# Optimization experiments

Measured on AMD Instinct MI355X. Metric: run time of the kernel, lower is better.

## Reference

```python
import jax, jax.numpy as jnp
import numpy as np

N = 40000          # nodes
E = 640000         # edges (avg degree 16)
F_IN = 128         # num_node_features
H = 64             # hidden_channels
C_OUT = 32         # num_classes


def _glorot(key, fan_in, fan_out):
    lim = np.sqrt(6.0 / (fan_in + fan_out)).astype(np.float32)
    return jax.random.uniform(key, (fan_in, fan_out), jnp.float32, -lim, lim)


def setup_inputs() -> dict:
    key = jax.random.key(0)
    ks = jax.random.split(key, 12)
    x = jax.random.normal(ks[0], (N, F_IN), jnp.float32)
    edge_index = jax.random.randint(ks[1], (2, E), 0, N, dtype=jnp.int32)
    batch = jnp.zeros((N,), jnp.int32)  # unused by forward, kept for signature fidelity
    return {
        "x": x,
        "edge_index": edge_index,
        "batch": batch,
        "W1": _glorot(ks[2], F_IN, H),      "b1": jnp.zeros((H,), jnp.float32),
        "W2": _glorot(ks[3], H, 2 * H),     "b2": jnp.zeros((2 * H,), jnp.float32),
        "W3": _glorot(ks[4], 2 * H, 2 * H), "b3": jnp.zeros((2 * H,), jnp.float32),
        "W4": _glorot(ks[5], 2 * H, H),     "b4": jnp.zeros((H,), jnp.float32),
        "Wl": _glorot(ks[6], H, C_OUT),     "bl": jnp.zeros((C_OUT,), jnp.float32),
    }


def _gcn_norm(edge_index, n_nodes):
    """Add self-loops and compute symmetric D^{-1/2} A D^{-1/2} edge weights."""
    loop = jnp.arange(n_nodes, dtype=edge_index.dtype)
    src = jnp.concatenate([edge_index[0], loop])
    dst = jnp.concatenate([edge_index[1], loop])
    deg = jax.ops.segment_sum(jnp.ones_like(dst, dtype=jnp.float32), dst,
                              num_segments=n_nodes)
    d_inv_sqrt = jnp.where(deg > 0, jax.lax.rsqrt(deg), 0.0)
    norm = d_inv_sqrt[src] * d_inv_sqrt[dst]  # [E + N]
    return src, dst, norm


def _gcn_conv(h, W, b, src, dst, norm, n_nodes):
    h = h @ W                                   # [N, d_out] linear transform first
    msg = h[src] * norm[:, None]                # gather + edge scaling
    agg = jax.ops.segment_sum(msg, dst, num_segments=n_nodes)  # scatter-add
    return agg + b


def reference(x, edge_index, batch, W1, b1, W2, b2, W3, b3, W4, b4, Wl, bl):
    n_nodes = x.shape[0]
    src, dst, norm = _gcn_norm(edge_index, n_nodes)
    # eval mode: F.dropout(training=False) is identity
    h = jax.nn.relu(_gcn_conv(x, W1, b1, src, dst, norm, n_nodes))
    h = jax.nn.relu(_gcn_conv(h, W2, b2, src, dst, norm, n_nodes))
    h = jax.nn.relu(_gcn_conv(h, W3, b3, src, dst, norm, n_nodes))
    h = jax.nn.relu(_gcn_conv(h, W4, b4, src, dst, norm, n_nodes))
    return h @ Wl + bl  # [N, C_OUT]
```

## Files before the change

### kernel.cpp

```cpp
#include <hip/hip_runtime.h>
#include <hip/hip_bf16.h>


using bf16x8 = __attribute__((ext_vector_type(8))) __bf16;
using f32x4  = __attribute__((ext_vector_type(4))) float;

#define BUKCAP 8192

__device__ __forceinline__ int block_detect_bf16(const unsigned short* __restrict__ x16) {
    __shared__ int cnt;
    if (threadIdx.x == 0) cnt = 0;
    __syncthreads();
    if (threadIdx.x < 128) {
        unsigned e = (x16[2 * threadIdx.x] >> 7) & 0xFF;
        if (e >= 100 && e <= 135) atomicAdd(&cnt, 1);
    }
    __syncthreads();
    return cnt >= 64;
}

struct PrepDesc { const void* src; void* dst; int n; int mode; int dol2; int strideK; };
struct PrepArgs { PrepDesc d[12]; int pre[13]; int ndesc; };

__global__ __launch_bounds__(256) void prep_stage(PrepArgs a,
// ... 8 lines not shown
    const int npre = a.pre[a.ndesc];
    if (b >= npre) {
        __shared__ int hist[160], start[160], run[160];
        const int t = threadIdx.x;
        const int base = (b - npre) * 2048;
        int sv[8], dv[8];
        #pragma unroll
        for (int j = 0; j < 8; ++j) {
            int e = base + j * 256 + t;
            if (e < E) { sv[j] = src[e]; dv[j] = dst[e]; } else dv[j] = -1;
        }
        if (t < NBUK) { hist[t] = 0; run[t] = 0; }
        __syncthreads();
        #pragma unroll
        for (int j = 0; j < 8; ++j)
            if (dv[j] >= 0) atomicAdd(&hist[dv[j] >> 8], 1);
        __syncthreads();
        if (t < NBUK && hist[t] > 0)
            start[t] = atomicAdd(&bukFill[t], hist[t]);
        __syncthreads();
        #pragma unroll
        for (int j = 0; j < 8; ++j) {
            if (dv[j] >= 0) {
                int bk = dv[j] >> 8;
                int slot = start[bk] + atomicAdd(&run[bk], 1);
                staging[(size_t)bk * BUKCAP + slot] = ((unsigned)dv[j] << 16) | (unsigned)sv[j];
            }
        }
        return;
    }
    const int fl = block_detect_bf16(x16);
    if (b == 0 && threadIdx.x == 0) *flagG = fl;
    int s = 0;
    for (; s < a.ndesc - 1; ++s) if (b < a.pre[s + 1]) break;
    const PrepDesc d = a.d[s];
    int i = (b - a.pre[s]) * 256 + threadIdx.x;
    if (i >= d.n) return;
    float v = fl ? __bfloat162float(((const __hip_bfloat16*)d.src)[i])
                 : ((const float*)d.src)[i];
    if (d.mode == 0) {
        ((float*)d.dst)[i] = v;
    } else {
        int k = i >> d.dol2;
        int col = i & ((1 << d.dol2) - 1);
        ((__hip_bfloat16*)d.dst)[col * d.strideK + k] = __float2bfloat16(v);
    }
}

template<int NTPW, bool RAW_A>
__device__ __forceinline__ void gemm_core(const void* __restrict__ Ain,
                                          const __hip_bfloat16* __restrict__ WT,
                                          __hip_bfloat16* __restrict__ out,
                                          int d_in, int d_out_log2, int strideK,
                                          bool bfmode, int blk, int tid) {
    const int wave = tid >> 6, lane = tid & 63;
    const int m = lane & 15, quad = lane >> 4;
    const int rowBase = blk * 64;
    const int nkc = d_in >> 5;
    const int nt0 = wave * NTPW;

    f32x4 acc[4][NTPW];
    #pragma unroll
    for (int rt = 0; rt < 4; ++rt)
        #pragma unroll
        for (int j = 0; j < NTPW; ++j)
            acc[rt][j] = (f32x4){0.f, 0.f, 0.f, 0.f};

    auto mainloop = [&](bool asBF) {
        for (int kc = 0; kc < nkc; ++kc) {
            const int koff = (kc << 5) + quad * 8;
            bf16x8 a[4];
            #pragma unroll
            for (int rt = 0; rt < 4; ++rt) {
                const size_t off = (size_t)(rowBase + rt * 16 + m) * d_in + koff;
                if (!RAW_A || asBF) {
                    a[rt] = *(const bf16x8*)((const __hip_bfloat16*)Ain + off);
                } else {
                    const float* p = (const float*)Ain + off;
                    float4 f0 = *(const float4*)p;
                    float4 f1 = *(const float4*)(p + 4);
                    union { bf16x8 v; __hip_bfloat16 h[8]; } u;
                    u.h[0] = __float2bfloat16(f0.x); u.h[1] = __float2bfloat16(f0.y);
                    u.h[2] = __float2bfloat16(f0.z); u.h[3] = __float2bfloat16(f0.w);
                    u.h[4] = __float2bfloat16(f1.x); u.h[5] = __float2bfloat16(f1.y);
                    u.h[6] = __float2bfloat16(f1.z); u.h[7] = __float2bfloat16(f1.w);
                    a[rt] = u.v;
                }
            }
            #pragma unroll
            for (int j = 0; j < NTPW; ++j) {
                const int n = ((nt0 + j) << 4) + m;
                bf16x8 b = *(const bf16x8*)&WT[n * strideK + koff];
                #pragma unroll
                for (int rt = 0; rt < 4; ++rt)
                    acc[rt][j] = __builtin_amdgcn_mfma_f32_16x16x32_bf16(a[rt], b, acc[rt][j], 0, 0, 0);
            }
        }
    };
    if (bfmode) mainloop(true); else mainloop(false);

    const int d_out = 1 << d_out_log2;
    #pragma unroll
    for (int rt = 0; rt < 4; ++rt) {
        const int row = rowBase + rt * 16 + quad * 4;
        #pragma unroll
        for (int j = 0; j < NTPW; ++j) {
            const int col = ((nt0 + j) << 4) + m;
            #pragma unroll
            for (int r = 0; r < 4; ++r)
                out[(size_t)(row + r) * d_out + col] = __float2bfloat16(acc[rt][j][r]);
        }
    }
}

__global__ __launch_bounds__(256) void scatter_gemm(const unsigned* __restrict__ staging,
                                                    const int* __restrict__ bukFill,
                                                    float* __restrict__ dinvA,
                                                    int2* __restrict__ nodeInfo,
                                                    unsigned short* __restrict__ csr16,
                                                    int N, int NBUK,
                                                    const void* __restrict__ x,
                                                    const __hip_bfloat16* __restrict__ WT0,
                                                    __hip_bfloat16* __restrict__ lin1,
                                                    int strideK0,
                                                    const int* __restrict__ flag,
                                                    __hip_bfloat16* __restrict__ TbufS,
                                                    __hip_bfloat16* __restrict__ HbufS) {
    if ((int)blockIdx.x < NBUK) {
        __shared__ int cur[256];
        const int t = threadIdx.x;
        const int i = (blockIdx.x << 8) + t;
        cur[t] = i * 64;
        if ((int)blockIdx.x == NBUK - 1) {
            if (i == N) dinvA[N] = 0.f;
            unsigned* z1 = (unsigned*)(TbufS + (size_t)N * 64);
            unsigned* z2 = (unsigned*)(TbufS + (size_t)N * 128);
            unsigned* z3 = (unsigned*)(HbufS + (size_t)N * 64);
            if (t < 32) z1[t] = 0u;
            else if (t < 96) z2[t - 32] = 0u;
            else if (t < 128) z3[t - 96] = 0u;
        }
        __syncthreads();
        const int fill = bukFill[blockIdx.x];
        const unsigned* st = staging + (size_t)blockIdx.x * BUKCAP;
        for (int k = t; k < fill; k += 256) {
            unsigned u = st[k];
            int pos = atomicAdd(&cur[(u >> 16) & 255], 1);
            csr16[pos] = (unsigned short)(u & 0xffffu);
        }
        __syncthreads();
        const int c = cur[t] - i * 64;
        const int cp = (c + 7) & ~7;
        if (i < N) {
            const float dv = rsqrtf((float)(c + 1));
            nodeInfo[i] = make_int2(__float_as_int(dv), cp);
            dinvA[i] = dv;
        }
        const int e1 = i * 64 + cp;
        for (int p = cur[t]; p < e1; ++p) csr16[p] = (unsigned short)N;
        return;
    }
    gemm_core<1, true>(x, WT0, lin1, 128, 6, strideK0,
                       (*flag != 0), blockIdx.x - NBUK, threadIdx.x);
}

template<int W>
__device__ __forceinline__ float gather_acc8w(const __hip_bfloat16* __restrict__ Hin,
                                              int cb, int node,
                                              const int2* __restrict__ nodeInfo,
                                              const unsigned short* __restrict__ csr16,
                                              const float* __restrict__ dinvA,
                                              float acc[8]) {
    const __hip_bfloat16* base = Hin + cb;
    const unsigned short* wp = csr16 + (size_t)node * 64;
    uint4 ix0 = *(const uint4*)(wp);
    uint4 ix1 = *(const uint4*)(wp + 8);
    const uint4 selfv = *(const uint4*)(base + (size_t)node * W);
    const int2 info = nodeInfo[node];
    const float di = __int_as_float(info.x);
    const int cp = info.y;
    auto loadrow = [&](unsigned s) -> uint4 {
        return *(const uint4*)(base + (size_t)s * W);
    };
    auto accumw = [&](uint4 v, float w) {
        union { uint4 q; __hip_bfloat162 h2[4]; } c;
        c.q = v;
        #pragma unroll
        for (int j = 0; j < 4; ++j) {
            float2 p = __bfloat1622float2(c.h2[j]);
            acc[2 * j]     += w * p.x;
            acc[2 * j + 1] += w * p.y;
        }
    };
    #pragma unroll
    for (int j = 0; j < 8; ++j) acc[j] = 0.f;
    accumw(selfv, di);
    int e = 0;
    uint4 cu = ix0, nx = ix1;
    while (e < cp) {
        const unsigned s0 = cu.x & 0xffffu, s1 = cu.x >> 16;
        const unsigned s2 = cu.y & 0xffffu, s3 = cu.y >> 16;
        const unsigned s4 = cu.z & 0xffffu, s5 = cu.z >> 16;
        const unsigned s6 = cu.w & 0xffffu, s7 = cu.w >> 16;
        uint4 r0 = loadrow(s0), r1 = loadrow(s1), r2 = loadrow(s2), r3 = loadrow(s3);
        uint4 r4 = loadrow(s4), r5 = loadrow(s5), r6 = loadrow(s6), r7 = loadrow(s7);
        float w0 = dinvA[s0], w1 = dinvA[s1], w2 = dinvA[s2], w3 = dinvA[s3];
        float w4 = dinvA[s4], w5 = dinvA[s5], w6 = dinvA[s6], w7 = dinvA[s7];
        uint4 pf = (e + 16 < cp) ? *(const uint4*)(wp + e + 16) : nx;
        accumw(r0, w0); accumw(r1, w1); accumw(r2, w2); accumw(r3, w3);
        accumw(r4, w4); accumw(r5, w5); accumw(r6, w6); accumw(r7, w7);
        cu = nx; nx = pf;
        e += 8;
    }
    return di;
}

__global__ __launch_bounds__(256) void gather8(const __hip_bfloat16* __restrict__ Hin,
                                               const int2* __restrict__ nodeInfo,
                                               const unsigned short* __restrict__ csr16,
                                               const float* __restrict__ dinvA,
                                               const float* __restrict__ b,
                                               __hip_bfloat16* __restrict__ out, int n) {
    const int t = blockIdx.x * 256 + threadIdx.x;
    const int node = t >> 3;
    const int f = t & 7;
    if (node >= n) return;
    const int cb = f * 8;
    float acc[8];
    const float di = gather_acc8w<64>(Hin, cb, node, nodeInfo, csr16, dinvA, acc);
    union { uint4 v; __hip_bfloat16 h[8]; } p;
    #pragma unroll
    for (int j = 0; j < 8; ++j)
        p.h[j] = __float2bfloat16(fmaxf(di * acc[j] + b[cb + j], 0.f));
    *(uint4*)(out + (size_t)node * 64 + cb) = p.v;
}

template<int D_IN, int NTPW>
__global__ __launch_bounds__(256) void gather_gemm(const __hip_bfloat16* __restrict__ Hin,
                                                   const int2* __restrict__ nodeInfo,
                                                   const unsigned short* __restrict__ csr16,
                                                   const float* __restrict__ dinvA,
                                                   const __hip_bfloat16* __restrict__ WT,
                                                   const float* __restrict__ bias,
                                                   __hip_bfloat16* __restrict__ out,
                                                   int d_out_log2) {
    constexpr int SK = D_IN + 8;
    __shared__ __align__(16) __hip_bfloat16 sG[64 * SK];
    const int tid = threadIdx.x;
    const int rowBase = blockIdx.x * 64;
    constexpr int TPR = D_IN / 8;
    constexpr int NPP = 256 / TPR;
    #pragma unroll
    for (int pass = 0; pass < 64 / NPP; ++pass) {
        const int local = pass * NPP + tid / TPR;
        const int node = rowBase + local;
        const int cb = (tid % TPR) * 8;
        float acc[8];
        const float di = gather_acc8w<D_IN>(Hin, cb, node, nodeInfo, csr16, dinvA, acc);
        union { bf16x8 v; __hip_bfloat16 h[8]; } p;
        #pragma unroll
        for (int j = 0; j < 8; ++j) p.h[j] = __float2bfloat16(di * acc[j]);
        *(bf16x8*)&sG[local * SK + cb] = p.v;
    }
    __syncthreads();

    const int wave = tid >> 6, lane = tid & 63;
    const int m = lane & 15, quad = lane >> 4;
    const int nkc = D_IN >> 5;
    const int nt0 = wave * NTPW;

    f32x4 acc2[4][NTPW];
    #pragma unroll
    for (int rt = 0; rt < 4; ++rt)
        #pragma unroll
        for (int j = 0; j < NTPW; ++j)
            acc2[rt][j] = (f32x4){0.f, 0.f, 0.f, 0.f};

    for (int kc = 0; kc < nkc; ++kc) {
        const int koff = (kc << 5) + quad * 8;
        bf16x8 a[4];
        #pragma unroll
        for (int rt = 0; rt < 4; ++rt)
            a[rt] = *(const bf16x8*)&sG[(rt * 16 + m) * SK + koff];
        #pragma unroll
        for (int j = 0; j < NTPW; ++j) {
            const int n = ((nt0 + j) << 4) + m;
            bf16x8 b = *(const bf16x8*)&WT[n * SK + koff];
            #pragma unroll
            for (int rt = 0; rt < 4; ++rt)
                acc2[rt][j] = __builtin_amdgcn_mfma_f32_16x16x32_bf16(a[rt], b, acc2[rt][j], 0, 0, 0);
        }
    }

    const int d_out = 1 << d_out_log2;
    #pragma unroll
    for (int rt = 0; rt < 4; ++rt) {
        const int row = rowBase + rt * 16 + quad * 4;
        #pragma unroll
        for (int j = 0; j < NTPW; ++j) {
            const int col = ((nt0 + j) << 4) + m;
            const float bv = bias[col];
            #pragma unroll
            for (int r = 0; r < 4; ++r)
                out[(size_t)(row + r) * d_out + col] =
                    __float2bfloat16(fmaxf(acc2[rt][j][r] + bv, 0.f));
        }
    }
}

__global__ __launch_bounds__(256) void gather_gemm34(const __hip_bfloat16* __restrict__ Hin,
                                                     const int2* __restrict__ nodeInfo,
                                                     const unsigned short* __restrict__ csr16,
                                                     const float* __restrict__ dinvA,
                                                     const __hip_bfloat16* __restrict__ WT3,
                                                     const float* __restrict__ b3,
                                                     const __hip_bfloat16* __restrict__ WT4,
                                                     __hip_bfloat16* __restrict__ lin4) {
    constexpr int SK = 136;
    __shared__ __align__(16) __hip_bfloat16 sG[64 * SK];
    const int tid = threadIdx.x;
    const int rowBase = blockIdx.x * 64;

    #pragma unroll
    for (int pass = 0; pass < 4; ++pass) {
        const int local = pass * 16 + tid / 16;
        const int node = rowBase + local;
        const int cb = (tid % 16) * 8;
        float acc[8];
        const float di = gather_acc8w<128>(Hin, cb, node, nodeInfo, csr16, dinvA, acc);
        union { bf16x8 v; __hip_bfloat16 h[8]; } p;
        #pragma unroll
        for (int j = 0; j < 8; ++j) p.h[j] = __float2bfloat16(di * acc[j]);
        *(bf16x8*)&sG[local * SK + cb] = p.v;
    }
    __syncthreads();

    const int wave = tid >> 6, lane = tid & 63;
    const int m = lane & 15, quad = lane >> 4;

    f32x4 acc2[4][2];
    #pragma unroll
    for (int rt = 0; rt < 4; ++rt)
        #pragma unroll
        for (int j = 0; j < 2; ++j)
            acc2[rt][j] = (f32x4){0.f, 0.f, 0.f, 0.f};
    for (int kc = 0; kc < 4; ++kc) {
        const int koff = (kc << 5) + quad * 8;
        bf16x8 a[4];
        #pragma unroll
        for (int rt = 0; rt < 4; ++rt)
            a[rt] = *(const bf16x8*)&sG[(rt * 16 + m) * SK + koff];
        #pragma unroll
        for (int j = 0; j < 2; ++j) {
            const int n = ((wave * 2 + j) << 4) + m;
            bf16x8 b = *(const bf16x8*)&WT3[n * SK + koff];
            #pragma unroll
            for (int rt = 0; rt < 4; ++rt)
                acc2[rt][j] = __builtin_amdgcn_mfma_f32_16x16x32_bf16(a[rt], b, acc2[rt][j], 0, 0, 0);
        }
    }
    __syncthreads();

    #pragma unroll
    for (int j = 0; j < 2; ++j) {
        const int col = ((wave * 2 + j) << 4) + m;
        const float bv = b3[col];
        #pragma unroll
        for (int rt = 0; rt < 4; ++rt) {
            const int row = rt * 16 + quad * 4;
            #pragma unroll
            for (int r = 0; r < 4; ++r)
                sG[(row + r) * SK + col] = __float2bfloat16(fmaxf(acc2[rt][j][r] + bv, 0.f));
        }
    }
    __syncthreads();

    f32x4 acc3[4];
    #pragma unroll
    for (int rt = 0; rt < 4; ++rt) acc3[rt] = (f32x4){0.f, 0.f, 0.f, 0.f};
    for (int kc = 0; kc < 4; ++kc) {
        const int koff = (kc << 5) + quad * 8;
        bf16x8 a[4];
        #pragma unroll
        for (int rt = 0; rt < 4; ++rt)
            a[rt] = *(const bf16x8*)&sG[(rt * 16 + m) * SK + koff];
        const int n = (wave << 4) + m;
        bf16x8 b = *(const bf16x8*)&WT4[n * SK + koff];
        #pragma unroll
        for (int rt = 0; rt < 4; ++rt)
            acc3[rt] = __builtin_amdgcn_mfma_f32_16x16x32_bf16(a[rt], b, acc3[rt], 0, 0, 0);
    }
    const int col = (wave << 4) + m;
    #pragma unroll
    for (int rt = 0; rt < 4; ++rt) {
        const int row = rowBase + rt * 16 + quad * 4;
        #pragma unroll
        for (int r = 0; r < 4; ++r)
            lin4[(size_t)(row + r) * 64 + col] = __float2bfloat16(acc3[rt][r]);
    }
}

__global__ __launch_bounds__(512) void gather_final(const __hip_bfloat16* __restrict__ Hin,
                                                    const int2* __restrict__ nodeInfo,
                                                    const unsigned short* __restrict__ csr16,
                                                    const float* __restrict__ dinvA,
                                                    const float* __restrict__ b4,
                                                    const float* __restrict__ Wlf,
                                                    const float* __restrict__ blf,
                                                    void* __restrict__ out,
                                                    const int* __restrict__ flag) {
    __shared__ float sWl[64 * 32];
    __shared__ float sH[64 * 65];
    const int tid = threadIdx.x;
    ((float4*)sWl)[tid] = ((const float4*)Wlf)[tid];
    const int nl = tid >> 3, j = tid & 7, cb = j * 8;
    const int node = blockIdx.x * 64 + nl;
    float acc[8];
    const float di = gather_acc8w<64>(Hin, cb, node, nodeInfo, csr16, dinvA, acc);
    #pragma unroll
    for (int k = 0; k < 8; ++k)
        sH[nl * 65 + cb + k] = fmaxf(di * acc[k] + b4[cb + k], 0.f);
    __syncthreads();
    float4 r = *(const float4*)(blf + 4 * j);
    for (int k = 0; k < 64; ++k) {
        const float hv = sH[nl * 65 + k];
        const float4 w = *(const float4*)&sWl[k * 32 + 4 * j];
        r.x += hv * w.x; r.y += hv * w.y; r.z += hv * w.z; r.w += hv * w.w;
    }
    const size_t idx = (size_t)node * 32 + 4 * j;
    if (*flag) {
        union { __hip_bfloat16 h[4]; uint2 u; } p;
        p.h[0] = __float2bfloat16(r.x); p.h[1] = __float2bfloat16(r.y);
        p.h[2] = __float2bfloat16(r.z); p.h[3] = __float2bfloat16(r.w);
        *(uint2*)((__hip_bfloat16*)out + idx) = p.u;
    } else {
        *(float4*)((float*)out + idx) = r;
    }
}

extern "C" void kernel_launch(void* const* d_in, const int* in_sizes, int n_in,
                              void* d_out, int out_size, void* d_ws, size_t ws_size,
                              hipStream_t stream) {
    const int* edge = (const int*)d_in[1];
    const int F_IN = 128;
    const int N = in_sizes[0] / F_IN;
    const int E = in_sizes[1] / 2;
    const int* src = edge;
    const int* dst = edge + E;
    const int NBUK = (N + 255) >> 8;

    auto align256 = [](size_t v) { return (v + 255) & ~(size_t)255; };
    char* ws = (char*)d_ws;
    int*   flag     = (int*)ws;    ws += 256;
    float* dinvA    = (float*)ws;  ws += align256((size_t)(N + 1) * 4);
    int2*  nodeInfo = (int2*)ws;   ws += align256((size_t)N * 8);
    int*   bukFill  = (int*)ws;    ws += align256((size_t)NBUK * 4);
    unsigned short* csr16 = (unsigned short*)ws; ws += align256((size_t)N * 64 * 2);
    unsigned* staging = (unsigned*)ws; ws += align256((size_t)NBUK * BUKCAP * 4);
    __hip_bfloat16* Hbuf = (__hip_bfloat16*)ws; ws += align256((size_t)(N + 2) * 128 * 2);
    __hip_bfloat16* Tbuf = (__hip_bfloat16*)ws; ws += align256((size_t)(N + 2) * 128 * 2);

    const int widx[4] = {3, 5, 7, 9};
    const int bidx[4] = {4, 6, 8, 10};
    float* Bc[4];
    for (int i = 0; i < 4; ++i) { Bc[i] = (float*)ws; ws += align256((size_t)in_sizes[bidx[i]] * 4); }
    float* Wlf = (float*)ws; ws += align256((size_t)in_sizes[11] * 4);
    float* blf = (float*)ws; ws += align256((size_t)in_sizes[12] * 4);

    const int LD_IN[4]  = {128, 64, 128, 128};
    const int LD_OL2[4] = {6, 7, 7, 6};
    int strideK[4];
    __hip_bfloat16* WT[4];
    for (int l = 0; l < 4; ++l) {
        strideK[l] = LD_IN[l] + 8;
        WT[l] = (__hip_bfloat16*)ws;
        ws += align256((size_t)(1 << LD_OL2[l]) * strideK[l] * 2);
    }

    hipMemsetAsync(bukFill, 0, (size_t)NBUK * 4, stream);

    PrepArgs pa{};
    int nd = 0, pre = 0;
    auto addDesc = [&](const void* s, void* d, int n, int mode, int dol2, int sk) {
        pa.d[nd] = {s, d, n, mode, dol2, sk};
        pa.pre[nd] = pre;
        pre += (n + 255) / 256;
        nd++;
    };
    for (int l = 0; l < 4; ++l)
        addDesc(d_in[widx[l]], WT[l], LD_IN[l] << LD_OL2[l], 1, LD_OL2[l], strideK[l]);
    for (int l = 0; l < 4; ++l)
        addDesc(d_in[bidx[l]], Bc[l], in_sizes[bidx[l]], 0, 0, 0);
    addDesc(d_in[11], Wlf, in_sizes[11], 0, 0, 0);
    addDesc(d_in[12], blf, in_sizes[12], 0, 0, 0);
    pa.pre[nd] = pre;
    pa.ndesc = nd;
    const int SB = (E + 2047) / 2048;
    prep_stage<<<pre + SB, 256, 0, stream>>>(pa, (const unsigned short*)d_in[0], flag,
                                             src, dst, E, NBUK, bukFill, staging);

    const int nblk = N / 64;
    const int g64  = (N * 8 + 255) / 256;

    scatter_gemm<<<NBUK + nblk, 256, 0, stream>>>(staging, bukFill, dinvA, nodeInfo, csr16,
                                                  N, NBUK, d_in[0], WT[0], Tbuf, strideK[0],
                                                  flag, Tbuf, Hbuf);

    gather8<<<g64, 256, 0, stream>>>(Tbuf, nodeInfo, csr16, dinvA, Bc[0], Hbuf, N);

    gather_gemm<64, 2><<<nblk, 256, 0, stream>>>(Hbuf, nodeInfo, csr16, dinvA, WT[1], Bc[1], Tbuf, 7);

    gather_gemm34<<<nblk, 256, 0, stream>>>(Tbuf, nodeInfo, csr16, dinvA, WT[2], Bc[2], WT[3], Hbuf);

    gather_final<<<N / 64, 512, 0, stream>>>(Hbuf, nodeInfo, csr16, dinvA, Bc[3], Wlf, blf, d_out, flag);
}
```

Before: 193.7 us.

## Split fused gather+GEMM kernels into separate column-sliced gather and GEMM passes

Unfuses the neighbour aggregation from the MFMA GEMMs in layers 2-4 and the final linear. Aggregation now runs in a generic gather kernel that tiles 64 nodes per block and splits feature columns into 32-wide slices across blocks. Each GEMM reads the aggregated rows from a new intermediate buffer. The aim is more parallelism and better gather locality per block, and less LDS and register pressure from fusion, at the cost of extra global round-trips for the intermediates and more kernel launches.

```diff
diff --git a/kernel.cpp b/kernel.cpp
--- a/kernel.cpp
+++ b/kernel.cpp
@@ -84,7 +84,8 @@
                                           const __hip_bfloat16* __restrict__ WT,
                                           __hip_bfloat16* __restrict__ out,
                                           int d_in, int d_out_log2, int strideK,
-                                          bool bfmode, int blk, int tid) {
+                                          bool bfmode, int blk, int tid,
+                                          const float* __restrict__ bias, bool dorelu) {
     const int wave = tid >> 6, lane = tid & 63;
     const int m = lane & 15, quad = lane >> 4;
     const int rowBase = blk * 64;
@@ -138,9 +139,13 @@
         #pragma unroll
         for (int j = 0; j < NTPW; ++j) {
             const int col = ((nt0 + j) << 4) + m;
+            const float bv = bias ? bias[col] : 0.f;
             #pragma unroll
-            for (int r = 0; r < 4; ++r)
-                out[(size_t)(row + r) * d_out + col] = __float2bfloat16(acc[rt][j][r]);
+            for (int r = 0; r < 4; ++r) {
+                float v = acc[rt][j][r] + bv;
+                if (dorelu) v = fmaxf(v, 0.f);
+                out[(size_t)(row + r) * d_out + col] = __float2bfloat16(v);
+            }
         }
     }
 }
@@ -193,7 +198,7 @@
         return;
     }
     gemm_core<1, true>(x, WT0, lin1, 128, 6, strideK0,
-                       (*flag != 0), blockIdx.x - NBUK, threadIdx.x);
+                       (*flag != 0), blockIdx.x - NBUK, threadIdx.x, nullptr, false);
 }
 
 template<int W>
@@ -247,107 +252,47 @@
     return di;
 }
 
-__global__ __launch_bounds__(256) void gather8(const __hip_bfloat16* __restrict__ Hin,
+template<int W, int LOG2S, bool BIASRELU>
+__global__ __launch_bounds__(256) void gatherS(const __hip_bfloat16* __restrict__ Hin,
                                                const int2* __restrict__ nodeInfo,
                                                const unsigned short* __restrict__ csr16,
                                                const float* __restrict__ dinvA,
                                                const float* __restrict__ b,
-                                               __hip_bfloat16* __restrict__ out, int n) {
-    const int t = blockIdx.x * 256 + threadIdx.x;
-    const int node = t >> 3;
-    const int f = t & 7;
-    if (node >= n) return;
-    const int cb = f * 8;
+                                               __hip_bfloat16* __restrict__ out) {
+    const int tid = threadIdx.x;
+    const int slice = blockIdx.x & ((1 << LOG2S) - 1);
+    const int nb = blockIdx.x >> LOG2S;
+    const int node = nb * 64 + (tid >> 2);
+    const int cb = slice * 32 + (tid & 3) * 8;
     float acc[8];
-    const float di = gather_acc8w<64>(Hin, cb, node, nodeInfo, csr16, dinvA, acc);
+    const float di = gather_acc8w<W>(Hin, cb, node, nodeInfo, csr16, dinvA, acc);
     union { uint4 v; __hip_bfloat16 h[8]; } p;
-    #pragma unroll
-    for (int j = 0; j < 8; ++j)
-        p.h[j] = __float2bfloat16(fmaxf(di * acc[j] + b[cb + j], 0.f));
-    *(uint4*)(out + (size_t)node * 64 + cb) = p.v;
-}
-
-template<int D_IN, int NTPW>
-__global__ __launch_bounds__(256) void gather_gemm(const __hip_bfloat16* __restrict__ Hin,
-                                                   const int2* __restrict__ nodeInfo,
-                                                   const unsigned short* __restrict__ csr16,
-                                                   const float* __restrict__ dinvA,
-                                                   const __hip_bfloat16* __restrict__ WT,
-                                                   const float* __restrict__ bias,
-                                                   __hip_bfloat16* __restrict__ out,
-                                                   int d_out_log2) {
-    constexpr int SK = D_IN + 8;
-    __shared__ __align__(16) __hip_bfloat16 sG[64 * SK];
-    const int tid = threadIdx.x;
-    const int rowBase = blockIdx.x * 64;
-    constexpr int TPR = D_IN / 8;
-    constexpr int NPP = 256 / TPR;
-    #pragma unroll
-    for (int pass = 0; pass < 64 / NPP; ++pass) {
-        const int local = pass * NPP + tid / TPR;
-        const int node = rowBase + local;
-        const int cb = (tid % TPR) * 8;
-        float acc[8];
-        const float di = gather_acc8w<D_IN>(Hin, cb, node, nodeInfo, csr16, dinvA, acc);
-        union { bf16x8 v; __hip_bfloat16 h[8]; } p;
-        #pragma unroll
-        for (int j = 0; j < 8; ++j) p.h[j] = __float2bfloat16(di * acc[j]);
-        *(bf16x8*)&sG[local * SK + cb] = p.v;
-    }
-    __syncthreads();
-
-    const int wave = tid >> 6, lane = tid & 63;
-    const int m = lane & 15, quad = lane >> 4;
-    const int nkc = D_IN >> 5;
-    const int nt0 = wave * NTPW;
-
-    f32x4 acc2[4][NTPW];
-    #pragma unroll
-    for (int rt = 0; rt < 4; ++rt)
-        #pragma unroll
-        for (int j = 0; j < NTPW; ++j)
-            acc2[rt][j] = (f32x4){0.f, 0.f, 0.f, 0.f};
-
-    for (int kc = 0; kc < nkc; ++kc) {
-        const int koff = (kc << 5) + quad * 8;
-        bf16x8 a[4];
-        #pragma unroll
-        for (int rt = 0; rt < 4; ++rt)
-            a[rt] = *(const bf16x8*)&sG[(rt * 16 + m) * SK + koff];
-        #pragma unroll
-        for (int j = 0; j < NTPW; ++j) {
-            const int n = ((nt0 + j) << 4) + m;
-            bf16x8 b = *(const bf16x8*)&WT[n * SK + koff];
-            #pragma unroll
-            for (int rt = 0; rt < 4; ++rt)
-                acc2[rt][j] = __builtin_amdgcn_mfma_f32_16x16x32_bf16(a[rt], b, acc2[rt][j], 0, 0, 0);
-        }
-    }
-
-    const int d_out = 1 << d_out_log2;
-    #pragma unroll
-    for (int rt = 0; rt < 4; ++rt) {
-        const int row = rowBase + rt * 16 + quad * 4;
-        #pragma unroll
-        for (int j = 0; j < NTPW; ++j) {
-            const int col = ((nt0 + j) << 4) + m;
-            const float bv = bias[col];
-            #pragma unroll
-            for (int r = 0; r < 4; ++r)
-                out[(size_t)(row + r) * d_out + col] =
-                    __float2bfloat16(fmaxf(acc2[rt][j][r] + bv, 0.f));
-        }
-    }
-}
-
-__global__ __launch_bounds__(256) void gather_gemm34(const __hip_bfloat16* __restrict__ Hin,
-                                                     const int2* __restrict__ nodeInfo,
-                                                     const unsigned short* __restrict__ csr16,
-                                                     const float* __restrict__ dinvA,
-                                                     const __hip_bfloat16* __restrict__ WT3,
-                                                     const float* __restrict__ b3,
-                                                     const __hip_bfloat16* __restrict__ WT4,
-                                                     __hip_bfloat16* __restrict__ lin4) {
+    if constexpr (BIASRELU) {
+        #pragma unroll
+        for (int j = 0; j < 8; ++j)
+            p.h[j] = __float2bfloat16(fmaxf(di * acc[j] + b[cb + j], 0.f));
+    } else {
+        #pragma unroll
+        for (int j = 0; j < 8; ++j)
+            p.h[j] = __float2bfloat16(di * acc[j]);
+    }
+    *(uint4*)(out + (size_t)node * W + cb) = p.v;
+}
+
+__global__ __launch_bounds__(256) void gemm_l2(const __hip_bfloat16* __restrict__ A,
+                                               const __hip_bfloat16* __restrict__ WT,
+                                               const float* __restrict__ bias,
+                                               __hip_bfloat16* __restrict__ out,
+                                               int strideK) {
+    gemm_core<2, false>(A, WT, out, 64, 7, strideK, true,
+                        blockIdx.x, threadIdx.x, bias, true);
+}
+
+__global__ __launch_bounds__(256) void gemm34(const __hip_bfloat16* __restrict__ agg3,
+                                              const __hip_bfloat16* __restrict__ WT3,
+                                              const float* __restrict__ b3,
+                                              const __hip_bfloat16* __restrict__ WT4,
+                                              __hip_bfloat16* __restrict__ lin4) {
     constexpr int SK = 136;
     __shared__ __align__(16) __hip_bfloat16 sG[64 * SK];
     const int tid = threadIdx.x;
@@ -355,15 +300,10 @@
 
     #pragma unroll
     for (int pass = 0; pass < 4; ++pass) {
-        const int local = pass * 16 + tid / 16;
-        const int node = rowBase + local;
+        const int row = pass * 16 + tid / 16;
         const int cb = (tid % 16) * 8;
-        float acc[8];
-        const float di = gather_acc8w<128>(Hin, cb, node, nodeInfo, csr16, dinvA, acc);
-        union { bf16x8 v; __hip_bfloat16 h[8]; } p;
-        #pragma unroll
-        for (int j = 0; j < 8; ++j) p.h[j] = __float2bfloat16(di * acc[j]);
-        *(bf16x8*)&sG[local * SK + cb] = p.v;
+        *(bf16x8*)&sG[row * SK + cb] =
+            *(const bf16x8*)&agg3[(size_t)(rowBase + row) * 128 + cb];
     }
     __syncthreads();
 
@@ -432,11 +372,7 @@
     }
 }
 
-__global__ __launch_bounds__(512) void gather_final(const __hip_bfloat16* __restrict__ Hin,
-                                                    const int2* __restrict__ nodeInfo,
-                                                    const unsigned short* __restrict__ csr16,
-                                                    const float* __restrict__ dinvA,
-                                                    const float* __restrict__ b4,
+__global__ __launch_bounds__(512) void final_linear(const __hip_bfloat16* __restrict__ h5,
                                                     const float* __restrict__ Wlf,
                                                     const float* __restrict__ blf,
                                                     void* __restrict__ out,
@@ -447,11 +383,14 @@
     ((float4*)sWl)[tid] = ((const float4*)Wlf)[tid];
     const int nl = tid >> 3, j = tid & 7, cb = j * 8;
     const int node = blockIdx.x * 64 + nl;
-    float acc[8];
-    const float di = gather_acc8w<64>(Hin, cb, node, nodeInfo, csr16, dinvA, acc);
-    #pragma unroll
-    for (int k = 0; k < 8; ++k)
-        sH[nl * 65 + cb + k] = fmaxf(di * acc[k] + b4[cb + k], 0.f);
+    union { uint4 q; __hip_bfloat162 h2[4]; } c;
+    c.q = *(const uint4*)(h5 + (size_t)node * 64 + cb);
+    #pragma unroll
+    for (int k = 0; k < 4; ++k) {
+        float2 p = __bfloat1622float2(c.h2[k]);
+        sH[nl * 65 + cb + 2 * k]     = p.x;
+        sH[nl * 65 + cb + 2 * k + 1] = p.y;
+    }
     __syncthreads();
     float4 r = *(const float4*)(blf + 4 * j);
     for (int k = 0; k < 64; ++k) {
@@ -491,6 +430,7 @@
     unsigned* staging = (unsigned*)ws; ws += align256((size_t)NBUK * BUKCAP * 4);
     __hip_bfloat16* Hbuf = (__hip_bfloat16*)ws; ws += align256((size_t)(N + 2) * 128 * 2);
     __hip_bfloat16* Tbuf = (__hip_bfloat16*)ws; ws += align256((size_t)(N + 2) * 128 * 2);
+    __hip_bfloat16* Abuf = (__hip_bfloat16*)ws; ws += align256((size_t)(N + 2) * 128 * 2);
 
     const int widx[4] = {3, 5, 7, 9};
     const int bidx[4] = {4, 6, 8, 10};
@@ -532,17 +472,22 @@
                                              src, dst, E, NBUK, bukFill, staging);
 
     const int nblk = N / 64;
-    const int g64  = (N * 8 + 255) / 256;
 
     scatter_gemm<<<NBUK + nblk, 256, 0, stream>>>(staging, bukFill, dinvA, nodeInfo, csr16,
                                                   N, NBUK, d_in[0], WT[0], Tbuf, strideK[0],
                                                   flag, Tbuf, Hbuf);
 
-    gather8<<<g64, 256, 0, stream>>>(Tbuf, nodeInfo, csr16, dinvA, Bc[0], Hbuf, N);
-
-    gather_gemm<64, 2><<<nblk, 256, 0, stream>>>(Hbuf, nodeInfo, csr16, dinvA, WT[1], Bc[1], Tbuf, 7);
-
-    gather_gemm34<<<nblk, 256, 0, stream>>>(Tbuf, nodeInfo, csr16, dinvA, WT[2], Bc[2], WT[3], Hbuf);
-
-    gather_final<<<N / 64, 512, 0, stream>>>(Hbuf, nodeInfo, csr16, dinvA, Bc[3], Wlf, blf, d_out, flag);
-}
+    gatherS<64, 1, true><<<nblk * 2, 256, 0, stream>>>(Tbuf, nodeInfo, csr16, dinvA, Bc[0], Hbuf);
+
+    gatherS<64, 1, false><<<nblk * 2, 256, 0, stream>>>(Hbuf, nodeInfo, csr16, dinvA, nullptr, Abuf);
+
+    gemm_l2<<<nblk, 256, 0, stream>>>(Abuf, WT[1], Bc[1], Tbuf, strideK[1]);
+
+    gatherS<128, 2, false><<<nblk * 4, 256, 0, stream>>>(Tbuf, nodeInfo, csr16, dinvA, nullptr, Abuf);
+
+    gemm34<<<nblk, 256, 0, stream>>>(Abuf, WT[2], Bc[2], WT[3], Hbuf);
+
+    gatherS<64, 1, true><<<nblk * 2, 256, 0, stream>>>(Hbuf, nodeInfo, csr16, dinvA, Bc[3], Abuf);
+
+    final_linear<<<nblk, 512, 0, stream>>>(Abuf, Wlf, blf, d_out, flag);
+}
```

Result: slower. 239.3 us (+23.5%).

## Pack source index and bf16 edge weight into 32-bit CSR for later gathers

Applied to the files above, without the earlier changes.

The first gather kernel now also writes a packed 32-bit CSR whose entries hold the source index in the low half and the bf16-rounded dinv of the source in the high half. The later three gather layers read this packed array, so they no longer do a dependent dinvA lookup per edge. The gather loops are also restructured to software-pipeline the next 8 neighbor row loads ahead of the accumulation. The cost is an extra N*64*4-byte array, extra padding writes in the scatter stage, and bf16 rounding of the edge weights, which changes precision slightly.

```diff
diff --git a/kernel.cpp b/kernel.cpp
--- a/kernel.cpp
+++ b/kernel.cpp
@@ -150,6 +150,7 @@
                                                     float* __restrict__ dinvA,
                                                     int2* __restrict__ nodeInfo,
                                                     unsigned short* __restrict__ csr16,
+                                                    unsigned* __restrict__ csr32,
                                                     int N, int NBUK,
                                                     const void* __restrict__ x,
                                                     const __hip_bfloat16* __restrict__ WT0,
@@ -181,85 +182,167 @@
             csr16[pos] = (unsigned short)(u & 0xffffu);
         }
         __syncthreads();
-        const int c = cur[t] - i * 64;
-        const int cp = (c + 7) & ~7;
         if (i < N) {
+            const int c = cur[t] - i * 64;
+            const int cp = (c + 7) & ~7;
             const float dv = rsqrtf((float)(c + 1));
             nodeInfo[i] = make_int2(__float_as_int(dv), cp);
             dinvA[i] = dv;
-        }
-        const int e1 = i * 64 + cp;
-        for (int p = cur[t]; p < e1; ++p) csr16[p] = (unsigned short)N;
+            const int e1 = i * 64 + 64;
+            for (int p = cur[t]; p < e1; ++p) {
+                csr16[p] = (unsigned short)N;
+                csr32[p] = (unsigned)N;
+            }
+        }
         return;
     }
     gemm_core<1, true>(x, WT0, lin1, 128, 6, strideK0,
                        (*flag != 0), blockIdx.x - NBUK, threadIdx.x);
 }
 
-template<int W>
-__device__ __forceinline__ float gather_acc8w(const __hip_bfloat16* __restrict__ Hin,
-                                              int cb, int node,
-                                              const int2* __restrict__ nodeInfo,
-                                              const unsigned short* __restrict__ csr16,
-                                              const float* __restrict__ dinvA,
-                                              float acc[8]) {
+__device__ __forceinline__ void accum8(float acc[8], uint4 v, float w) {
+    union { uint4 q; __hip_bfloat162 h2[4]; } c;
+    c.q = v;
+    #pragma unroll
+    for (int j = 0; j < 4; ++j) {
+        float2 p = __bfloat1622float2(c.h2[j]);
+        acc[2 * j]     += w * p.x;
+        acc[2 * j + 1] += w * p.y;
+    }
+}
+
+__device__ __forceinline__ float gather_pack64(const __hip_bfloat16* __restrict__ Hin,
+                                               int cb, int node, int f,
+                                               const int2* __restrict__ nodeInfo,
+                                               const unsigned short* __restrict__ csr16,
+                                               const float* __restrict__ dinvA,
+                                               unsigned* __restrict__ csr32,
+                                               float acc[8]) {
     const __hip_bfloat16* base = Hin + cb;
     const unsigned short* wp = csr16 + (size_t)node * 64;
-    uint4 ix0 = *(const uint4*)(wp);
-    uint4 ix1 = *(const uint4*)(wp + 8);
+    unsigned* op = csr32 + (size_t)node * 64;
+    uint4 c0 = *(const uint4*)(wp);
+    uint4 c1 = *(const uint4*)(wp + 8);
+    const uint4 selfv = *(const uint4*)(base + (size_t)node * 64);
+    const int2 info = nodeInfo[node];
+    const float di = __int_as_float(info.x);
+    const int cp = info.y;
+    auto loadrow = [&](unsigned s) -> uint4 {
+        return *(const uint4*)(base + (size_t)s * 64);
+    };
+    #pragma unroll
+    for (int j = 0; j < 8; ++j) acc[j] = 0.f;
+
+    unsigned s[8], sn[8];
+    float w[8], wn[8];
+    uint4 r[8], n[8];
+    s[0] = c0.x & 0xffffu; s[1] = c0.x >> 16;
+    s[2] = c0.y & 0xffffu; s[3] = c0.y >> 16;
+    s[4] = c0.z & 0xffffu; s[5] = c0.z >> 16;
+    s[6] = c0.w & 0xffffu; s[7] = c0.w >> 16;
+    #pragma unroll
+    for (int j = 0; j < 8; ++j) { r[j] = loadrow(s[j]); w[j] = dinvA[s[j]]; }
+    accum8(acc, selfv, di);
+    int e = 0;
+    while (true) {
+        const bool more = (e + 8) < cp;
+        const int pe = (e + 16) <= 56 ? (e + 16) : 56;
+        uint4 pf = *(const uint4*)(wp + pe);
+        if (more) {
+            sn[0] = c1.x & 0xffffu; sn[1] = c1.x >> 16;
+            sn[2] = c1.y & 0xffffu; sn[3] = c1.y >> 16;
+            sn[4] = c1.z & 0xffffu; sn[5] = c1.z >> 16;
+            sn[6] = c1.w & 0xffffu; sn[7] = c1.w >> 16;
+            #pragma unroll
+            for (int j = 0; j < 8; ++j) { n[j] = loadrow(sn[j]); wn[j] = dinvA[sn[j]]; }
+        }
+        unsigned pk = 0;
+        #pragma unroll
+        for (int j = 0; j < 8; ++j) {
+            union { __hip_bfloat16 h; unsigned short b; } cv;
+            cv.h = __float2bfloat16(w[j]);
+            unsigned pkj = ((unsigned)cv.b << 16) | s[j];
+            if (f == j) pk = pkj;
+        }
+        op[e + f] = pk;
+        #pragma unroll
+        for (int j = 0; j < 8; ++j) accum8(acc, r[j], w[j]);
+        if (!more) break;
+        c0 = c1; c1 = pf;
+        #pragma unroll
+        for (int j = 0; j < 8; ++j) { s[j] = sn[j]; w[j] = wn[j]; r[j] = n[j]; }
+        e += 8;
+    }
+    return di;
+}
+
+template<int W>
+__device__ __forceinline__ float gather_p32(const __hip_bfloat16* __restrict__ Hin,
+                                            int cb, int node,
+                                            const int2* __restrict__ nodeInfo,
+                                            const unsigned* __restrict__ csr32,
+                                            float acc[8]) {
+    const __hip_bfloat16* base = Hin + cb;
+    const unsigned* wp = csr32 + (size_t)node * 64;
+    uint4 ea0 = *(const uint4*)(wp);
+    uint4 eb0 = *(const uint4*)(wp + 4);
+    uint4 ea1 = *(const uint4*)(wp + 8);
+    uint4 eb1 = *(const uint4*)(wp + 12);
     const uint4 selfv = *(const uint4*)(base + (size_t)node * W);
     const int2 info = nodeInfo[node];
     const float di = __int_as_float(info.x);
     const int cp = info.y;
-    auto loadrow = [&](unsigned s) -> uint4 {
-        return *(const uint4*)(base + (size_t)s * W);
+    auto loadrow = [&](unsigned u) -> uint4 {
+        return *(const uint4*)(base + (size_t)(u & 0xffffu) * W);
     };
-    auto accumw = [&](uint4 v, float w) {
-        union { uint4 q; __hip_bfloat162 h2[4]; } c;
-        c.q = v;
-        #pragma unroll
-        for (int j = 0; j < 4; ++j) {
-            float2 p = __bfloat1622float2(c.h2[j]);
-            acc[2 * j]     += w * p.x;
-            acc[2 * j + 1] += w * p.y;
-        }
+    auto wof = [](unsigned u) -> float {
+        return __int_as_float((int)(u & 0xffff0000u));
     };
     #pragma unroll
     for (int j = 0; j < 8; ++j) acc[j] = 0.f;
-    accumw(selfv, di);
+    uint4 r[8], n[8];
+    r[0] = loadrow(ea0.x); r[1] = loadrow(ea0.y); r[2] = loadrow(ea0.z); r[3] = loadrow(ea0.w);
+    r[4] = loadrow(eb0.x); r[5] = loadrow(eb0.y); r[6] = loadrow(eb0.z); r[7] = loadrow(eb0.w);
+    accum8(acc, selfv, di);
     int e = 0;
-    uint4 cu = ix0, nx = ix1;
-    while (e < cp) {
-        const unsigned s0 = cu.x & 0xffffu, s1 = cu.x >> 16;
-        const unsigned s2 = cu.y & 0xffffu, s3 = cu.y >> 16;
-        const unsigned s4 = cu.z & 0xffffu, s5 = cu.z >> 16;
-        const unsigned s6 = cu.w & 0xffffu, s7 = cu.w >> 16;
-        uint4 r0 = loadrow(s0), r1 = loadrow(s1), r2 = loadrow(s2), r3 = loadrow(s3);
-        uint4 r4 = loadrow(s4), r5 = loadrow(s5), r6 = loadrow(s6), r7 = loadrow(s7);
-        float w0 = dinvA[s0], w1 = dinvA[s1], w2 = dinvA[s2], w3 = dinvA[s3];
-        float w4 = dinvA[s4], w5 = dinvA[s5], w6 = dinvA[s6], w7 = dinvA[s7];
-        uint4 pf = (e + 16 < cp) ? *(const uint4*)(wp + e + 16) : nx;
-        accumw(r0, w0); accumw(r1, w1); accumw(r2, w2); accumw(r3, w3);
-        accumw(r4, w4); accumw(r5, w5); accumw(r6, w6); accumw(r7, w7);
-        cu = nx; nx = pf;
+    while (true) {
+        const bool more = (e + 8) < cp;
+        const int pe = (e + 16) <= 56 ? (e + 16) : 56;
+        uint4 pa = *(const uint4*)(wp + pe);
+        uint4 pb = *(const uint4*)(wp + pe + 4);
+        if (more) {
+            n[0] = loadrow(ea1.x); n[1] = loadrow(ea1.y);
+            n[2] = loadrow(ea1.z); n[3] = loadrow(ea1.w);
+            n[4] = loadrow(eb1.x); n[5] = loadrow(eb1.y);
+            n[6] = loadrow(eb1.z); n[7] = loadrow(eb1.w);
+        }
+        accum8(acc, r[0], wof(ea0.x)); accum8(acc, r[1], wof(ea0.y));
+        accum8(acc, r[2], wof(ea0.z)); accum8(acc, r[3], wof(ea0.w));
+        accum8(acc, r[4], wof(eb0.x)); accum8(acc, r[5], wof(eb0.y));
+        accum8(acc, r[6], wof(eb0.z)); accum8(acc, r[7], wof(eb0.w));
+        if (!more) break;
+        ea0 = ea1; eb0 = eb1; ea1 = pa; eb1 = pb;
+        #pragma unroll
+        for (int j = 0; j < 8; ++j) r[j] = n[j];
         e += 8;
     }
     return di;
 }
 
-__global__ __launch_bounds__(256) void gather8(const __hip_bfloat16* __restrict__ Hin,
-                                               const int2* __restrict__ nodeInfo,
-                                               const unsigned short* __restrict__ csr16,
-                                               const float* __restrict__ dinvA,
-                                               const float* __restrict__ b,
-                                               __hip_bfloat16* __restrict__ out, int n) {
+__global__ __launch_bounds__(256) void gather8_pack(const __hip_bfloat16* __restrict__ Hin,
+                                                    const int2* __restrict__ nodeInfo,
+                                                    const unsigned short* __restrict__ csr16,
+                                                    const float* __restrict__ dinvA,
+                                                    unsigned* __restrict__ csr32,
+                                                    const float* __restrict__ b,
+                                                    __hip_bfloat16* __restrict__ out, int n) {
     const int t = blockIdx.x * 256 + threadIdx.x;
     const int node = t >> 3;
     const int f = t & 7;
     if (node >= n) return;
     const int cb = f * 8;
     float acc[8];
-    const float di = gather_acc8w<64>(Hin, cb, node, nodeInfo, csr16, dinvA, acc);
+    const float di = gather_pack64(Hin, cb, node, f, nodeInfo, csr16, dinvA, csr32, acc);
     union { uint4 v; __hip_bfloat16 h[8]; } p;
     #pragma unroll
     for (int j = 0; j < 8; ++j)
@@ -270,8 +353,7 @@
 template<int D_IN, int NTPW>
 __global__ __launch_bounds__(256) void gather_gemm(const __hip_bfloat16* __restrict__ Hin,
                                                    const int2* __restrict__ nodeInfo,
-                                                   const unsigned short* __restrict__ csr16,
-                                                   const float* __restrict__ dinvA,
+                                                   const unsigned* __restrict__ csr32,
                                                    const __hip_bfloat16* __restrict__ WT,
                                                    const float* __restrict__ bias,
                                                    __hip_bfloat16* __restrict__ out,
@@ -288,7 +370,7 @@
         const int node = rowBase + local;
         const int cb = (tid % TPR) * 8;
         float acc[8];
-        const float di = gather_acc8w<D_IN>(Hin, cb, node, nodeInfo, csr16, dinvA, acc);
+        const float di = gather_p32<D_IN>(Hin, cb, node, nodeInfo, csr32, acc);
         union { bf16x8 v; __hip_bfloat16 h[8]; } p;
         #pragma unroll
         for (int j = 0; j < 8; ++j) p.h[j] = __float2bfloat16(di * acc[j]);
@@ -342,8 +424,7 @@
 
 __global__ __launch_bounds__(256) void gather_gemm34(const __hip_bfloat16* __restrict__ Hin,
                                                      const int2* __restrict__ nodeInfo,
-                                                     const unsigned short* __restrict__ csr16,
-                                                     const float* __restrict__ dinvA,
+                                                     const unsigned* __restrict__ csr32,
                                                      const __hip_bfloat16* __restrict__ WT3,
                                                      const float* __restrict__ b3,
                                                      const __hip_bfloat16* __restrict__ WT4,
@@ -359,7 +440,7 @@
         const int node = rowBase + local;
         const int cb = (tid % 16) * 8;
         float acc[8];
-        const float di = gather_acc8w<128>(Hin, cb, node, nodeInfo, csr16, dinvA, acc);
+        const float di = gather_p32<128>(Hin, cb, node, nodeInfo, csr32, acc);
         union { bf16x8 v; __hip_bfloat16 h[8]; } p;
         #pragma unroll
         for (int j = 0; j < 8; ++j) p.h[j] = __float2bfloat16(di * acc[j]);
@@ -434,8 +515,7 @@
 
 __global__ __launch_bounds__(512) void gather_final(const __hip_bfloat16* __restrict__ Hin,
                                                     const int2* __restrict__ nodeInfo,
-                                                    const unsigned short* __restrict__ csr16,
-                                                    const float* __restrict__ dinvA,
+                                                    const unsigned* __restrict__ csr32,
                                                     const float* __restrict__ b4,
                                                     const float* __restrict__ Wlf,
                                                     const float* __restrict__ blf,
@@ -448,7 +528,7 @@
     const int nl = tid >> 3, j = tid & 7, cb = j * 8;
     const int node = blockIdx.x * 64 + nl;
     float acc[8];
-    const float di = gather_acc8w<64>(Hin, cb, node, nodeInfo, csr16, dinvA, acc);
+    const float di = gather_p32<64>(Hin, cb, node, nodeInfo, csr32, acc);
     #pragma unroll
     for (int k = 0; k < 8; ++k)
         sH[nl * 65 + cb + k] = fmaxf(di * acc[k] + b4[cb + k], 0.f);
@@ -488,6 +568,7 @@
     int2*  nodeInfo = (int2*)ws;   ws += align256((size_t)N * 8);
     int*   bukFill  = (int*)ws;    ws += align256((size_t)NBUK * 4);
     unsigned short* csr16 = (unsigned short*)ws; ws += align256((size_t)N * 64 * 2);
+    unsigned* csr32 = (unsigned*)ws; ws += align256((size_t)N * 64 * 4);
     unsigned* staging = (unsigned*)ws; ws += align256((size_t)NBUK * BUKCAP * 4);
     __hip_bfloat16* Hbuf = (__hip_bfloat16*)ws; ws += align256((size_t)(N + 2) * 128 * 2);
     __hip_bfloat16* Tbuf = (__hip_bfloat16*)ws; ws += align256((size_t)(N + 2) * 128 * 2);
@@ -535,14 +616,14 @@
     const int g64  = (N * 8 + 255) / 256;
 
     scatter_gemm<<<NBUK + nblk, 256, 0, stream>>>(staging, bukFill, dinvA, nodeInfo, csr16,
-                                                  N, NBUK, d_in[0], WT[0], Tbuf, strideK[0],
-                                                  flag, Tbuf, Hbuf);
-
-    gather8<<<g64, 256, 0, stream>>>(Tbuf, nodeInfo, csr16, dinvA, Bc[0], Hbuf, N);
-
-    gather_gemm<64, 2><<<nblk, 256, 0, stream>>>(Hbuf, nodeInfo, csr16, dinvA, WT[1], Bc[1], Tbuf, 7);
-
-    gather_gemm34<<<nblk, 256, 0, stream>>>(Tbuf, nodeInfo, csr16, dinvA, WT[2], Bc[2], WT[3], Hbuf);
-
-    gather_final<<<N / 64, 512, 0, stream>>>(Hbuf, nodeInfo, csr16, dinvA, Bc[3], Wlf, blf, d_out, flag);
-}
+                                                  csr32, N, NBUK, d_in[0], WT[0], Tbuf,
+                                                  strideK[0], flag, Tbuf, Hbuf);
+
+    gather8_pack<<<g64, 256, 0, stream>>>(Tbuf, nodeInfo, csr16, dinvA, csr32, Bc[0], Hbuf, N);
+
+    gather_gemm<64, 2><<<nblk, 256, 0, stream>>>(Hbuf, nodeInfo, csr32, WT[1], Bc[1], Tbuf, 7);
+
+    gather_gemm34<<<nblk, 256, 0, stream>>>(Tbuf, nodeInfo, csr32, WT[2], Bc[2], WT[3], Hbuf);
+
+    gather_final<<<N / 64, 512, 0, stream>>>(Hbuf, nodeInfo, csr32, Bc[3], Wlf, blf, d_out, flag);
+}
```

Measured after the change: 208.1 us. 7.5% more time.

## Pack bf16 source weights into 32-bit CSR entries for later gather layers

Applied to the files above, without the earlier changes.

Adds a second CSR array where each edge entry holds the source index in its low 16 bits and that source's bf16 normalisation factor in its high 16 bits. The array is built by extra blocks inside the first gather launch. Layers 2-4 then read the weight from the packed word instead of doing a dependent dinvA load per edge, trading a doubled index-stream footprint and bf16-rounded weights for fewer scattered loads. It also clamps the prefetch offset to stay inside the 64-slot row and guards padding writes by i<N.

```diff
diff --git a/kernel.cpp b/kernel.cpp
--- a/kernel.cpp
+++ b/kernel.cpp
@@ -181,19 +181,30 @@
             csr16[pos] = (unsigned short)(u & 0xffffu);
         }
         __syncthreads();
-        const int c = cur[t] - i * 64;
-        const int cp = (c + 7) & ~7;
         if (i < N) {
+            const int c = cur[t] - i * 64;
+            const int cp = (c + 7) & ~7;
             const float dv = rsqrtf((float)(c + 1));
             nodeInfo[i] = make_int2(__float_as_int(dv), cp);
             dinvA[i] = dv;
-        }
-        const int e1 = i * 64 + cp;
-        for (int p = cur[t]; p < e1; ++p) csr16[p] = (unsigned short)N;
+            const int e1 = i * 64 + cp;
+            for (int p = cur[t]; p < e1; ++p) csr16[p] = (unsigned short)N;
+        }
         return;
     }
     gemm_core<1, true>(x, WT0, lin1, 128, 6, strideK0,
                        (*flag != 0), blockIdx.x - NBUK, threadIdx.x);
+}
+
+__device__ __forceinline__ void accum8(float acc[8], uint4 v, float w) {
+    union { uint4 q; __hip_bfloat162 h2[4]; } c;
+    c.q = v;
+    #pragma unroll
+    for (int j = 0; j < 4; ++j) {
+        float2 p = __bfloat1622float2(c.h2[j]);
+        acc[2 * j]     += w * p.x;
+        acc[2 * j + 1] += w * p.y;
+    }
 }
 
 template<int W>
@@ -214,19 +225,9 @@
     auto loadrow = [&](unsigned s) -> uint4 {
         return *(const uint4*)(base + (size_t)s * W);
     };
-    auto accumw = [&](uint4 v, float w) {
-        union { uint4 q; __hip_bfloat162 h2[4]; } c;
-        c.q = v;
-        #pragma unroll
-        for (int j = 0; j < 4; ++j) {
-            float2 p = __bfloat1622float2(c.h2[j]);
-            acc[2 * j]     += w * p.x;
-            acc[2 * j + 1] += w * p.y;
-        }
-    };
     #pragma unroll
     for (int j = 0; j < 8; ++j) acc[j] = 0.f;
-    accumw(selfv, di);
+    accum8(acc, selfv, di);
     int e = 0;
     uint4 cu = ix0, nx = ix1;
     while (e < cp) {
@@ -238,22 +239,96 @@
         uint4 r4 = loadrow(s4), r5 = loadrow(s5), r6 = loadrow(s6), r7 = loadrow(s7);
         float w0 = dinvA[s0], w1 = dinvA[s1], w2 = dinvA[s2], w3 = dinvA[s3];
         float w4 = dinvA[s4], w5 = dinvA[s5], w6 = dinvA[s6], w7 = dinvA[s7];
-        uint4 pf = (e + 16 < cp) ? *(const uint4*)(wp + e + 16) : nx;
-        accumw(r0, w0); accumw(r1, w1); accumw(r2, w2); accumw(r3, w3);
-        accumw(r4, w4); accumw(r5, w5); accumw(r6, w6); accumw(r7, w7);
+        uint4 pf = (e + 16 < cp) ? *(const uint4*)(wp + ((e + 16 <= 56) ? e + 16 : 56)) : nx;
+        accum8(acc, r0, w0); accum8(acc, r1, w1); accum8(acc, r2, w2); accum8(acc, r3, w3);
+        accum8(acc, r4, w4); accum8(acc, r5, w5); accum8(acc, r6, w6); accum8(acc, r7, w7);
         cu = nx; nx = pf;
         e += 8;
     }
     return di;
 }
 
-__global__ __launch_bounds__(256) void gather8(const __hip_bfloat16* __restrict__ Hin,
-                                               const int2* __restrict__ nodeInfo,
-                                               const unsigned short* __restrict__ csr16,
-                                               const float* __restrict__ dinvA,
-                                               const float* __restrict__ b,
-                                               __hip_bfloat16* __restrict__ out, int n) {
-    const int t = blockIdx.x * 256 + threadIdx.x;
+template<int W>
+__device__ __forceinline__ float gather_p32(const __hip_bfloat16* __restrict__ Hin,
+                                            int cb, int node,
+                                            const int2* __restrict__ nodeInfo,
+                                            const unsigned* __restrict__ csr32,
+                                            float acc[8]) {
+    const __hip_bfloat16* base = Hin + cb;
+    const unsigned* wp = csr32 + (size_t)node * 64;
+    uint4 ea = *(const uint4*)(wp);
+    uint4 eb = *(const uint4*)(wp + 4);
+    uint4 na = *(const uint4*)(wp + 8);
+    uint4 nb = *(const uint4*)(wp + 12);
+    const uint4 selfv = *(const uint4*)(base + (size_t)node * W);
+    const int2 info = nodeInfo[node];
+    const float di = __int_as_float(info.x);
+    const int cp = info.y;
+    auto loadrow = [&](unsigned u) -> uint4 {
+        return *(const uint4*)(base + (size_t)(u & 0xffffu) * W);
+    };
+    auto wof = [](unsigned u) -> float {
+        return __int_as_float((int)(u & 0xffff0000u));
+    };
+    #pragma unroll
+    for (int j = 0; j < 8; ++j) acc[j] = 0.f;
+    accum8(acc, selfv, di);
+    int e = 0;
+    while (e < cp) {
+        uint4 r0 = loadrow(ea.x), r1 = loadrow(ea.y), r2 = loadrow(ea.z), r3 = loadrow(ea.w);
+        uint4 r4 = loadrow(eb.x), r5 = loadrow(eb.y), r6 = loadrow(eb.z), r7 = loadrow(eb.w);
+        const int pe = (e + 16 <= 56) ? e + 16 : 56;
+        uint4 pa = *(const uint4*)(wp + pe);
+        uint4 pb = *(const uint4*)(wp + pe + 4);
+        accum8(acc, r0, wof(ea.x)); accum8(acc, r1, wof(ea.y));
+        accum8(acc, r2, wof(ea.z)); accum8(acc, r3, wof(ea.w));
+        accum8(acc, r4, wof(eb.x)); accum8(acc, r5, wof(eb.y));
+        accum8(acc, r6, wof(eb.z)); accum8(acc, r7, wof(eb.w));
+        ea = na; eb = nb; na = pa; nb = pb;
+        e += 8;
+    }
+    return di;
+}
+
+__global__ __launch_bounds__(256) void gather8_packw(const __hip_bfloat16* __restrict__ Hin,
+                                                     const int2* __restrict__ nodeInfo,
+                                                     const unsigned short* __restrict__ csr16,
+                                                     const float* __restrict__ dinvA,
+                                                     unsigned* __restrict__ csr32,
+                                                     const float* __restrict__ b,
+                                                     __hip_bfloat16* __restrict__ out,
+                                                     int n, int nblk1) {
+    if ((int)blockIdx.x >= nblk1) {
+        const int t = ((int)blockIdx.x - nblk1) * 256 + threadIdx.x;
+        const int node = t >> 3;
+        const int f = t & 7;
+        if (node >= n) return;
+        const int cp = nodeInfo[node].y;
+        const int e0 = f * 8;
+        const unsigned short* wp = csr16 + (size_t)node * 64;
+        uint4 c = *(const uint4*)(wp + e0);
+        unsigned s[8];
+        s[0] = c.x & 0xffffu; s[1] = c.x >> 16;
+        s[2] = c.y & 0xffffu; s[3] = c.y >> 16;
+        s[4] = c.z & 0xffffu; s[5] = c.z >> 16;
+        s[6] = c.w & 0xffffu; s[7] = c.w >> 16;
+        unsigned pk[8];
+        #pragma unroll
+        for (int j = 0; j < 8; ++j) {
+            if (e0 + j < cp) {
+                union { __hip_bfloat16 h; unsigned short w16; } cv;
+                cv.h = __float2bfloat16(dinvA[s[j]]);
+                pk[j] = ((unsigned)cv.w16 << 16) | s[j];
+            } else {
+                pk[j] = (unsigned)n;
+            }
+        }
+        unsigned* op = csr32 + (size_t)node * 64 + e0;
+        *(uint4*)(op)     = make_uint4(pk[0], pk[1], pk[2], pk[3]);
+        *(uint4*)(op + 4) = make_uint4(pk[4], pk[5], pk[6], pk[7]);
+        return;
+    }
+    const int t = (int)blockIdx.x * 256 + threadIdx.x;
     const int node = t >> 3;
     const int f = t & 7;
     if (node >= n) return;
@@ -270,8 +345,7 @@
 template<int D_IN, int NTPW>
 __global__ __launch_bounds__(256) void gather_gemm(const __hip_bfloat16* __restrict__ Hin,
                                                    const int2* __restrict__ nodeInfo,
-                                                   const unsigned short* __restrict__ csr16,
-                                                   const float* __restrict__ dinvA,
+                                                   const unsigned* __restrict__ csr32,
                                                    const __hip_bfloat16* __restrict__ WT,
                                                    const float* __restrict__ bias,
                                                    __hip_bfloat16* __restrict__ out,
@@ -288,7 +362,7 @@
         const int node = rowBase + local;
         const int cb = (tid % TPR) * 8;
         float acc[8];
-        const float di = gather_acc8w<D_IN>(Hin, cb, node, nodeInfo, csr16, dinvA, acc);
+        const float di = gather_p32<D_IN>(Hin, cb, node, nodeInfo, csr32, acc);
         union { bf16x8 v; __hip_bfloat16 h[8]; } p;
         #pragma unroll
         for (int j = 0; j < 8; ++j) p.h[j] = __float2bfloat16(di * acc[j]);
@@ -342,8 +416,7 @@
 
 __global__ __launch_bounds__(256) void gather_gemm34(const __hip_bfloat16* __restrict__ Hin,
                                                      const int2* __restrict__ nodeInfo,
-                                                     const unsigned short* __restrict__ csr16,
-                                                     const float* __restrict__ dinvA,
+                                                     const unsigned* __restrict__ csr32,
                                                      const __hip_bfloat16* __restrict__ WT3,
                                                      const float* __restrict__ b3,
                                                      const __hip_bfloat16* __restrict__ WT4,
@@ -359,7 +432,7 @@
         const int node = rowBase + local;
         const int cb = (tid % 16) * 8;
         float acc[8];
-        const float di = gather_acc8w<128>(Hin, cb, node, nodeInfo, csr16, dinvA, acc);
+        const float di = gather_p32<128>(Hin, cb, node, nodeInfo, csr32, acc);
         union { bf16x8 v; __hip_bfloat16 h[8]; } p;
         #pragma unroll
         for (int j = 0; j < 8; ++j) p.h[j] = __float2bfloat16(di * acc[j]);
@@ -434,8 +507,7 @@
 
 __global__ __launch_bounds__(512) void gather_final(const __hip_bfloat16* __restrict__ Hin,
                                                     const int2* __restrict__ nodeInfo,
-                                                    const unsigned short* __restrict__ csr16,
-                                                    const float* __restrict__ dinvA,
+                                                    const unsigned* __restrict__ csr32,
                                                     const float* __restrict__ b4,
                                                     const float* __restrict__ Wlf,
                                                     const float* __restrict__ blf,
@@ -448,7 +520,7 @@
     const int nl = tid >> 3, j = tid & 7, cb = j * 8;
     const int node = blockIdx.x * 64 + nl;
     float acc[8];
-    const float di = gather_acc8w<64>(Hin, cb, node, nodeInfo, csr16, dinvA, acc);
+    const float di = gather_p32<64>(Hin, cb, node, nodeInfo, csr32, acc);
     #pragma unroll
     for (int k = 0; k < 8; ++k)
         sH[nl * 65 + cb + k] = fmaxf(di * acc[k] + b4[cb + k], 0.f);
@@ -488,6 +560,7 @@
     int2*  nodeInfo = (int2*)ws;   ws += align256((size_t)N * 8);
     int*   bukFill  = (int*)ws;    ws += align256((size_t)NBUK * 4);
     unsigned short* csr16 = (unsigned short*)ws; ws += align256((size_t)N * 64 * 2);
+    unsigned* csr32 = (unsigned*)ws; ws += align256((size_t)N * 64 * 4);
     unsigned* staging = (unsigned*)ws; ws += align256((size_t)NBUK * BUKCAP * 4);
     __hip_bfloat16* Hbuf = (__hip_bfloat16*)ws; ws += align256((size_t)(N + 2) * 128 * 2);
     __hip_bfloat16* Tbuf = (__hip_bfloat16*)ws; ws += align256((size_t)(N + 2) * 128 * 2);
@@ -538,11 +611,12 @@
                                                   N, NBUK, d_in[0], WT[0], Tbuf, strideK[0],
                                                   flag, Tbuf, Hbuf);
 
-    gather8<<<g64, 256, 0, stream>>>(Tbuf, nodeInfo, csr16, dinvA, Bc[0], Hbuf, N);
-
-    gather_gemm<64, 2><<<nblk, 256, 0, stream>>>(Hbuf, nodeInfo, csr16, dinvA, WT[1], Bc[1], Tbuf, 7);
-
-    gather_gemm34<<<nblk, 256, 0, stream>>>(Tbuf, nodeInfo, csr16, dinvA, WT[2], Bc[2], WT[3], Hbuf);
-
-    gather_final<<<N / 64, 512, 0, stream>>>(Hbuf, nodeInfo, csr16, dinvA, Bc[3], Wlf, blf, d_out, flag);
-}
+    gather8_packw<<<g64 + g64, 256, 0, stream>>>(Tbuf, nodeInfo, csr16, dinvA, csr32,
+                                                 Bc[0], Hbuf, N, g64);
+
+    gather_gemm<64, 2><<<nblk, 256, 0, stream>>>(Hbuf, nodeInfo, csr32, WT[1], Bc[1], Tbuf, 7);
+
+    gather_gemm34<<<nblk, 256, 0, stream>>>(Tbuf, nodeInfo, csr32, WT[2], Bc[2], WT[3], Hbuf);
+
+    gather_final<<<N / 64, 512, 0, stream>>>(Hbuf, nodeInfo, csr32, Bc[3], Wlf, blf, d_out, flag);
+}
```

New measurement: 194.4 us. Within noise of the previous version (+0.4%).
